# Kernel tuning notes

Measured on AMD Instinct MI355X. Metric: run time of the kernel, lower is better.

The kernel has to match this reference:

```python
import jax, jax.numpy as jnp
import numpy as np

EPS = 1e-12

def _l2norm(x):
    # F.normalize(x, dim=1): x / max(||x||_2, eps)
    n = jnp.sqrt(jnp.sum(x * x, axis=1, keepdims=True))
    return x / jnp.maximum(n, EPS)

def setup_inputs() -> dict:
    key = jax.random.key(0)
    ks = jax.random.split(key, 8)
    n_users, n_entities, channel = 100000, 100000, 128
    n_edges, n_inter, n_rel_rows = 600000, 500000, 15
    return {
        "user_emb": jax.random.normal(ks[0], (n_users, channel), dtype=jnp.float32),
        "item_emb": jax.random.normal(ks[1], (n_entities, channel), dtype=jnp.float32) * 0.1,
        "edge_index": jax.random.randint(ks[2], (2, n_edges), 0, n_entities, dtype=jnp.int64),
        "edge_type": jax.random.randint(ks[3], (n_edges,), 1, n_rel_rows + 1, dtype=jnp.int64),
        "inter_edge": jnp.stack([
            jax.random.randint(ks[4], (n_inter,), 0, n_users, dtype=jnp.int64),
            jax.random.randint(ks[5], (n_inter,), 0, n_entities, dtype=jnp.int64),
        ]),
        "inter_edge_w": jax.random.uniform(ks[6], (n_inter,), dtype=jnp.float32),
        "relation_emb": jax.random.normal(ks[7], (n_rel_rows, channel), dtype=jnp.float32) * 0.1,
        "n_hops": 2,
    }

def reference(user_emb, item_emb, edge_index, edge_type, inter_edge, inter_edge_w, relation_emb, n_hops):
    head, tail = edge_index[0], edge_index[1]
    n_entities = item_emb.shape[0]
    n_users = user_emb.shape[0]

    ent = item_emb
    for _ in range(n_hops):
        he = ent[head]                       # [E, d] gather
        te = ent[tail]                       # [E, d] gather
        re = relation_emb[edge_type - 1]     # [E, d] gather
        # scores = exp(sum(h*r*t)) then scatter_softmax over head segments
        scores = jnp.exp(jnp.sum(he * re * te, axis=1))  # [E]
        smax = jax.ops.segment_max(scores, head, num_segments=n_entities)
        e = jnp.exp(scores - smax[head])
        denom = jax.ops.segment_sum(e, head, num_segments=n_entities)
        attn = e / denom[head]
        ent = jax.ops.segment_sum(attn[:, None] * te, head, num_segments=n_entities)
        # dropout in eval mode (identity), then F.normalize
        ent = _l2norm(ent)

    u_idx, i_idx = inter_edge[0], inter_edge[1]
    item_agg = inter_edge_w[:, None] * ent[i_idx]  # [Ninter, d]
    user_agg = jax.ops.segment_sum(item_agg, u_idx, num_segments=n_users)
    return (_l2norm(user_agg), ent)
```

## Files before the change

kernel.cpp:

```cpp
#include <hip/hip_runtime.h>
#include <math.h>

#define D 128
#define EPS 1e-12f
#define SCAN_NB 128
#define SCAN_TPB 256
#define CPAD 4

template <int CTRL>
__device__ __forceinline__ float rorAdd(float v) {
    int t = __builtin_amdgcn_update_dpp(0, __float_as_int(v), CTRL, 0xF, 0xF, true);
    return v + __int_as_float(t);
}
__device__ __forceinline__ float groupSum16(float v) {
    v = rorAdd<0x121>(v);
    v = rorAdd<0x122>(v);
    v = rorAdd<0x124>(v);
    v = rorAdd<0x128>(v);
    return v;
}

__device__ __forceinline__ void unpack8(uint4 q, float* f) {
    f[0] = __uint_as_float(q.x << 16); f[1] = __uint_as_float(q.x & 0xFFFF0000u);
    f[2] = __uint_as_float(q.y << 16); f[3] = __uint_as_float(q.y & 0xFFFF0000u);
    f[4] = __uint_as_float(q.z << 16); f[5] = __uint_as_float(q.z & 0xFFFF0000u);
    f[6] = __uint_as_float(q.w << 16); f[7] = __uint_as_float(q.w & 0xFFFF0000u);
}
__device__ __forceinline__ unsigned bfpack2(float lo, float hi) {
    unsigned ul = __float_as_uint(lo), uh = __float_as_uint(hi);
    ul = (ul + 0x7FFFu + ((ul >> 16) & 1u)) >> 16;
    uh = (uh + 0x7FFFu + ((uh >> 16) & 1u)) & 0xFFFF0000u;
    return ul | uh;
}
__device__ __forceinline__ uint4 pack8(const float* f) {
    uint4 q;
    q.x = bfpack2(f[0], f[1]); q.y = bfpack2(f[2], f[3]);
    q.z = bfpack2(f[4], f[5]); q.w = bfpack2(f[6], f[7]);
    return q;
}

__global__ void k_zero(int4* __restrict__ p, int n4) {
    int i = blockIdx.x * blockDim.x + threadIdx.x;
    if (i < n4) p[i] = make_int4(0, 0, 0, 0);
}

__global__ void k_count_conv(const int* __restrict__ head, const int* __restrict__ u_idx,
                             int* __restrict__ counts_pad, int* __restrict__ rank,
                             const float* __restrict__ emb, uint4* __restrict__ mir,
                             int E, int Ninter, int N_ent, int n8) {
    int i = blockIdx.x * blockDim.x + threadIdx.x;
    int n_keys = E + Ninter;
    if (i < E) {
        rank[i] = atomicAdd(&counts_pad[(size_t)head[i] << CPAD], 1);
    } else if (i < n_keys) {
        rank[i] = atomicAdd(&counts_pad[(size_t)(N_ent + u_idx[i - E]) << CPAD], 1);
    } else if (i < n_keys + n8) {
        int c = i - n_keys;
        const float4* ip = (const float4*)emb + (size_t)c * 2;
        float4 a = ip[0], b = ip[1];
        float f[8] = {a.x, a.y, a.z, a.w, b.x, b.y, b.z, b.w};
        mir[c] = pack8(f);
    }
}

__global__ void k_count_both(const int* __restrict__ head, const int* __restrict__ u_idx,
                             int* __restrict__ counts_all, int E, int Ninter, int N_ent) {
    int i = blockIdx.x * blockDim.x + threadIdx.x;
    if (i < E) atomicAdd(&counts_all[head[i]], 1);
    else if (i < E + Ninter) atomicAdd(&counts_all[N_ent + u_idx[i - E]], 1);
}

__global__ void k_scan_block(const int* __restrict__ counts, int* __restrict__ bsum,
                             int N, int K, int shl) {
    __shared__ int lds[SCAN_TPB];
    int tid = threadIdx.x;
    int base = (blockIdx.x * SCAN_TPB + tid) * K;
    int s = 0;
    for (int k = 0; k < K; ++k) {
        int idx = base + k;
        if (idx < N) s += counts[(size_t)idx << shl];
    }
    lds[tid] = s;
    __syncthreads();
    for (int off = SCAN_TPB / 2; off > 0; off >>= 1) {
        if (tid < off) lds[tid] += lds[tid + off];
        __syncthreads();
    }
    if (tid == 0) bsum[blockIdx.x] = lds[0];
}

__global__ void k_scan_top(int* __restrict__ bsum) {
    __shared__ int lds[SCAN_NB];
    int t = threadIdx.x;
    if (t < SCAN_NB) lds[t] = bsum[t];
    __syncthreads();
    if (t == 0) {
        int run = 0;
        for (int i = 0; i < SCAN_NB; ++i) { int c = lds[i]; lds[i] = run; run += c; }
    }
    __syncthreads();
    if (t < SCAN_NB) bsum[t] = lds[t];
}

__global__ void k_scan_final(const int* __restrict__ counts, const int* __restrict__ bsum,
                             int* __restrict__ row_start, int N, int K, int shl) {
    __shared__ int lds[SCAN_TPB];
    int tid = threadIdx.x;
    int base = (blockIdx.x * SCAN_TPB + tid) * K;
    int s = 0;
    for (int k = 0; k < K; ++k) {
        int idx = base + k;
        if (idx < N) s += counts[(size_t)idx << shl];
    }
    lds[tid] = s;
    __syncthreads();
    for (int off = 1; off < SCAN_TPB; off <<= 1) {
        int v = (tid >= off) ? lds[tid - off] : 0;
        __syncthreads();
        lds[tid] += v;
        __syncthreads();
    }
    int run = lds[tid] - s + bsum[blockIdx.x];
    for (int k = 0; k < K; ++k) {
        int idx = base + k;
        if (idx <= N) {
            row_start[idx] = run;
            if (idx < N) run += counts[(size_t)idx << shl];
        }
    }
}

__global__ void k_reorder_rank(const int* __restrict__ head, const int* __restrict__ tail,
                               const int* __restrict__ etype,
                               const int* __restrict__ u_idx, const int* __restrict__ i_idx,
                               const float* __restrict__ w,
                               const int* __restrict__ rs_all, const int* __restrict__ rank,
                               int* __restrict__ packed, int2* __restrict__ riw,
                               int E, int Ninter, int N_ent) {
    int i = blockIdx.x * blockDim.x + threadIdx.x;
    if (i < E) {
        int h = head[i];
        packed[rs_all[h] + rank[i]] = tail[i] | ((etype[i] - 1) << 24);
    } else if (i < E + Ninter) {
        int k = i - E;
        int u = N_ent + u_idx[k];
        int pos = rs_all[u] + rank[i] - E;
        riw[pos] = make_int2(i_idx[k], __float_as_int(w[k]));
    }
}

__global__ void k_reorder_both(const int* __restrict__ head, const int* __restrict__ tail,
                               const int* __restrict__ etype,
                               const int* __restrict__ u_idx, const int* __restrict__ i_idx,
                               const float* __restrict__ w,
                               const int* __restrict__ rs_all, int* __restrict__ cursor,
                               int* __restrict__ packed, int2* __restrict__ riw,
                               int E, int Ninter, int N_ent) {
    int i = blockIdx.x * blockDim.x + threadIdx.x;
    if (i < E) {
        int h = head[i];
        int pos = rs_all[h] + atomicAdd(&cursor[h], 1);
        packed[pos] = tail[i] | ((etype[i] - 1) << 24);
    } else if (i < E + Ninter) {
        int k = i - E;
        int u = N_ent + u_idx[k];
        int pos = rs_all[u] + atomicAdd(&cursor[u], 1) - E;
        riw[pos] = make_int2(i_idx[k], __float_as_int(w[k]));
    }
}

__global__ void k_hop_bf16(const uint4* __restrict__ ent16,
                           const float* __restrict__ rel,
                           const int* __restrict__ rs_all,
                           const int* __restrict__ packed,
                           float* __restrict__ out_f32,
                           uint4* __restrict__ out_bf16,
                           int N) {
    int lane = threadIdx.x & 63;
    int l16 = lane & 15;
    int row = ((blockIdx.x * blockDim.x + threadIdx.x) >> 6) * 4 + (lane >> 4);
    if (row >= N) return;

    int rs = rs_all[row];
    int deg = rs_all[row + 1] - rs;

    float hv[8];
    unpack8(ent16[(size_t)row * 16 + l16], hv);

    float acc[8] = {0, 0, 0, 0, 0, 0, 0, 0};
    if (deg > 0) {
        int p = packed[rs];
        uint4 t16 = ent16[(size_t)(p & 0xFFFFFF) * 16 + l16];
        const float4* rp = (const float4*)(rel + (size_t)(((unsigned)p) >> 24) * D);
        float4 ra = rp[l16 * 2], rb = rp[l16 * 2 + 1];
        for (int j = 0; j < deg; ++j) {
            uint4 ct16 = t16;
            float4 cra = ra, crb = rb;
            if (j + 1 < deg) {
                int pn = packed[rs + j + 1];
                t16 = ent16[(size_t)(pn & 0xFFFFFF) * 16 + l16];
                rp = (const float4*)(rel + (size_t)(((unsigned)pn) >> 24) * D);
                ra = rp[l16 * 2]; rb = rp[l16 * 2 + 1];
            }
            float tv[8];
            unpack8(ct16, tv);
            float v = hv[0] * cra.x * tv[0] + hv[1] * cra.y * tv[1] +
                      hv[2] * cra.z * tv[2] + hv[3] * cra.w * tv[3] +
                      hv[4] * crb.x * tv[4] + hv[5] * crb.y * tv[5] +
                      hv[6] * crb.z * tv[6] + hv[7] * crb.w * tv[7];
            v = groupSum16(v);
            float wgt = __expf(__expf(v));
#pragma unroll
            for (int k = 0; k < 8; ++k) acc[k] += wgt * tv[k];
        }
    }

    float part = 0.f;
#pragma unroll
    for (int k = 0; k < 8; ++k) part += acc[k] * acc[k];
    float ss = groupSum16(part);
    float inv = 1.0f / fmaxf(sqrtf(ss), EPS);
#pragma unroll
    for (int k = 0; k < 8; ++k) acc[k] *= inv;

    if (out_f32) {
        float4* op = (float4*)(out_f32 + (size_t)row * D);
        op[l16 * 2]     = make_float4(acc[0], acc[1], acc[2], acc[3]);
        op[l16 * 2 + 1] = make_float4(acc[4], acc[5], acc[6], acc[7]);
    }
    if (out_bf16) out_bf16[(size_t)row * 16 + l16] = pack8(acc);
}

__global__ void k_user_bf16(const uint4* __restrict__ ent16,
                            const int* __restrict__ rs_all,
                            const int2* __restrict__ riw,
                            float* __restrict__ uout, int Nu, int N_ent, int E) {
    int lane = threadIdx.x & 63;
    int l16 = lane & 15;
    int row = ((blockIdx.x * blockDim.x + threadIdx.x) >> 6) * 4 + (lane >> 4);
    if (row >= Nu) return;

    int base = rs_all[N_ent + row];
    int deg = rs_all[N_ent + row + 1] - base;
    int rs = base - E;

    float acc[8] = {0, 0, 0, 0, 0, 0, 0, 0};
    if (deg > 0) {
        int2 pw = riw[rs];
        uint4 t16 = ent16[(size_t)pw.x * 16 + l16];
        float ww = __int_as_float(pw.y);
        for (int j = 0; j < deg; ++j) {
            uint4 ct16 = t16;
            float cw = ww;
            if (j + 1 < deg) {
                int2 pn = riw[rs + j + 1];
                t16 = ent16[(size_t)pn.x * 16 + l16];
                ww = __int_as_float(pn.y);
            }
            float tv[8];
            unpack8(ct16, tv);
#pragma unroll
            for (int k = 0; k < 8; ++k) acc[k] += cw * tv[k];
        }
    }
    float part = 0.f;
#pragma unroll
    for (int k = 0; k < 8; ++k) part += acc[k] * acc[k];
    float ss = groupSum16(part);
    float inv = 1.0f / fmaxf(sqrtf(ss), EPS);
#pragma unroll
    for (int k = 0; k < 8; ++k) acc[k] *= inv;
    float4* op = (float4*)(uout + (size_t)row * D);
    op[l16 * 2]     = make_float4(acc[0], acc[1], acc[2], acc[3]);
    op[l16 * 2 + 1] = make_float4(acc[4], acc[5], acc[6], acc[7]);
}

__global__ void k_hop_f32(const float* __restrict__ ent_in,
                          const float* __restrict__ rel,
                          const int* __restrict__ rs_all,
                          const int* __restrict__ packed,
                          float* __restrict__ ent_out, int N) {
    int lane = threadIdx.x & 63;
    int l16 = lane & 15;
    int row = ((blockIdx.x * blockDim.x + threadIdx.x) >> 6) * 4 + (lane >> 4);
    if (row >= N) return;
    int rs = rs_all[row];
    int deg = rs_all[row + 1] - rs;
    const float4* hp = (const float4*)(ent_in + (size_t)row * D);
    float4 ha = hp[l16], hb = hp[l16 + 16];
    float4 acca = make_float4(0, 0, 0, 0), accb = make_float4(0, 0, 0, 0);
    for (int j = 0; j < deg; ++j) {
        int p = packed[rs + j];
        const float4* tp = (const float4*)(ent_in + (size_t)(p & 0xFFFFFF) * D);
        const float4* rp = (const float4*)(rel + (size_t)(((unsigned)p) >> 24) * D);
        float4 ta = tp[l16], tb = tp[l16 + 16];
        float4 ra = rp[l16], rb = rp[l16 + 16];
        float v = ha.x * ra.x * ta.x + ha.y * ra.y * ta.y +
                  ha.z * ra.z * ta.z + ha.w * ra.w * ta.w +
                  hb.x * rb.x * tb.x + hb.y * rb.y * tb.y +
                  hb.z * rb.z * tb.z + hb.w * rb.w * tb.w;
        v = groupSum16(v);
        float wgt = __expf(__expf(v));
        acca.x += wgt * ta.x; acca.y += wgt * ta.y;
        acca.z += wgt * ta.z; acca.w += wgt * ta.w;
        accb.x += wgt * tb.x; accb.y += wgt * tb.y;
        accb.z += wgt * tb.z; accb.w += wgt * tb.w;
    }
    float part = acca.x * acca.x + acca.y * acca.y + acca.z * acca.z + acca.w * acca.w +
                 accb.x * accb.x + accb.y * accb.y + accb.z * accb.z + accb.w * accb.w;
    float ss = groupSum16(part);
    float inv = 1.0f / fmaxf(sqrtf(ss), EPS);
    acca.x *= inv; acca.y *= inv; acca.z *= inv; acca.w *= inv;
    accb.x *= inv; accb.y *= inv; accb.z *= inv; accb.w *= inv;
    float4* op = (float4*)(ent_out + (size_t)row * D);
    op[l16] = acca;
    op[l16 + 16] = accb;
}

__global__ void k_user_f32(const float* __restrict__ ent,
                           const int* __restrict__ rs_all,
                           const int2* __restrict__ riw,
                           float* __restrict__ uout, int Nu, int N_ent, int E) {
    int lane = threadIdx.x & 63;
    int l16 = lane & 15;
    int row = ((blockIdx.x * blockDim.x + threadIdx.x) >> 6) * 4 + (lane >> 4);
    if (row >= Nu) return;
    int base = rs_all[N_ent + row];
    int deg = rs_all[N_ent + row + 1] - base;
    int rs = base - E;
    float4 acca = make_float4(0, 0, 0, 0), accb = make_float4(0, 0, 0, 0);
    for (int j = 0; j < deg; ++j) {
        int2 pw = riw[rs + j];
        float ww = __int_as_float(pw.y);
        const float4* ip = (const float4*)(ent + (size_t)pw.x * D);
        float4 ta = ip[l16], tb = ip[l16 + 16];
        acca.x += ww * ta.x; acca.y += ww * ta.y;
        acca.z += ww * ta.z; acca.w += ww * ta.w;
        accb.x += ww * tb.x; accb.y += ww * tb.y;
        accb.z += ww * tb.z; accb.w += ww * tb.w;
    }
    float part = acca.x * acca.x + acca.y * acca.y + acca.z * acca.z + acca.w * acca.w +
                 accb.x * accb.x + accb.y * accb.y + accb.z * accb.z + accb.w * accb.w;
    float ss = groupSum16(part);
    float inv = 1.0f / fmaxf(sqrtf(ss), EPS);
    acca.x *= inv; acca.y *= inv; acca.z *= inv; acca.w *= inv;
    accb.x *= inv; accb.y *= inv; accb.z *= inv; accb.w *= inv;
    float4* op = (float4*)(uout + (size_t)row * D);
    op[l16] = acca;
    op[l16 + 16] = accb;
}

extern "C" void kernel_launch(void* const* d_in, const int* in_sizes, int n_in,
                              void* d_out, int out_size, void* d_ws, size_t ws_size,
                              hipStream_t stream) {
    const float* item_emb  = (const float*)d_in[1];
    const int*   edge_idx  = (const int*)d_in[2];
    const int*   edge_type = (const int*)d_in[3];
    const int*   inter     = (const int*)d_in[4];
    const float* inter_w   = (const float*)d_in[5];
    const float* rel       = (const float*)d_in[6];

    const int N_users = in_sizes[0] / D;
    const int N_ent   = in_sizes[1] / D;
    const int E       = in_sizes[2] / 2;
    const int Ninter  = in_sizes[5];
    const int N_tot   = N_ent + N_users;
    const int n_keys  = E + Ninter;

    float* user_out = (float*)d_out;
    float* ent_out  = (float*)d_out + (size_t)N_users * D;

    const int* head  = edge_idx;
    const int* tail  = edge_idx + E;
    const int* u_idx = inter;
    const int* i_idx = inter + Ninter;

    const int TPB = 256;
    dim3 blk(TPB);

    const size_t mir_u4 = (size_t)N_ent * 16;
    const size_t cpad_n = (size_t)N_tot << CPAD;
    uint4* mirA     = (uint4*)d_ws;
    uint4* mirB     = mirA + mir_u4;
    int2* riw       = (int2*)(mirB + mir_u4);
    int* counts_pad = (int*)(riw + Ninter);
    int* rs_all     = counts_pad + cpad_n;
    int* packed     = rs_all + N_tot + 1;
    int* bsum       = packed + E;
    int* rank       = bsum + SCAN_NB;

    size_t ints_b   = ((size_t)Ninter * 2 + cpad_n + N_tot + 1 + E + SCAN_NB + n_keys) * 4;
    size_t need_b16 = mir_u4 * 2 * 16 + ints_b;
    bool use_b16 = ws_size >= need_b16;

    int K = (N_tot + SCAN_NB * SCAN_TPB - 1) / (SCAN_NB * SCAN_TPB);
    int n8 = N_ent * (D / 8);

    if (use_b16) {
        int n4p = (int)(cpad_n / 4);
        k_zero<<<(n4p + TPB - 1) / TPB, blk, 0, stream>>>((int4*)counts_pad, n4p);
        k_count_conv<<<(n_keys + n8 + TPB - 1) / TPB, blk, 0, stream>>>(
            head, u_idx, counts_pad, rank, item_emb, mirA, E, Ninter, N_ent, n8);
        k_scan_block<<<SCAN_NB, SCAN_TPB, 0, stream>>>(counts_pad, bsum, N_tot, K, CPAD);
        k_scan_top<<<1, SCAN_TPB, 0, stream>>>(bsum);
        k_scan_final<<<SCAN_NB, SCAN_TPB, 0, stream>>>(counts_pad, bsum, rs_all, N_tot, K, CPAD);
        k_reorder_rank<<<(n_keys + TPB - 1) / TPB, blk, 0, stream>>>(
            head, tail, edge_type, u_idx, i_idx, inter_w,
            rs_all, rank, packed, riw, E, Ninter, N_ent);

        int grid_rows  = (N_ent + 15) / 16;
        int grid_users = (N_users + 15) / 16;
        k_hop_bf16<<<grid_rows, blk, 0, stream>>>(
            mirA, rel, rs_all, packed, nullptr, mirB, N_ent);
        k_hop_bf16<<<grid_rows, blk, 0, stream>>>(
            mirB, rel, rs_all, packed, ent_out, mirA, N_ent);
        k_user_bf16<<<grid_users, blk, 0, stream>>>(
            mirA, rs_all, riw, user_out, N_users, N_ent, E);
    } else {
        int2* riw2       = (int2*)d_ws;
        int* counts_all  = (int*)(riw2 + Ninter);
        int* rs2         = counts_all + N_tot;
        int* packed2     = rs2 + N_tot + 1;
        int* bsum2       = packed2 + E;
        int n4 = N_tot / 4;
        k_zero<<<(n4 + TPB - 1) / TPB, blk, 0, stream>>>((int4*)counts_all, n4);
        k_count_both<<<(n_keys + TPB - 1) / TPB, blk, 0, stream>>>(
            head, u_idx, counts_all, E, Ninter, N_ent);
        k_scan_block<<<SCAN_NB, SCAN_TPB, 0, stream>>>(counts_all, bsum2, N_tot, K, 0);
        k_scan_top<<<1, SCAN_TPB, 0, stream>>>(bsum2);
        k_scan_final<<<SCAN_NB, SCAN_TPB, 0, stream>>>(counts_all, bsum2, rs2, N_tot, K, 0);
        k_zero<<<(n4 + TPB - 1) / TPB, blk, 0, stream>>>((int4*)counts_all, n4);
        k_reorder_both<<<(n_keys + TPB - 1) / TPB, blk, 0, stream>>>(
            head, tail, edge_type, u_idx, i_idx, inter_w,
            rs2, counts_all, packed2, riw2, E, Ninter, N_ent);
        int grid_rows  = (N_ent + 15) / 16;
        int grid_users = (N_users + 15) / 16;
        float* ent_mid = user_out;
        k_hop_f32<<<grid_rows, blk, 0, stream>>>(item_emb, rel, rs2, packed2, ent_mid, N_ent);
        k_hop_f32<<<grid_rows, blk, 0, stream>>>(ent_mid, rel, rs2, packed2, ent_out, N_ent);
        k_user_f32<<<grid_users, blk, 0, stream>>>(
            ent_out, rs2, riw2, user_out, N_users, N_ent, E);
    }
}
```

Measured before the change: 208.5 us.

## Split entity and user CSR builds and overlap user build with hop kernels

Result: no change. 209.7 us (+0.6%).

```diff
diff --git a/kernel.cpp b/kernel.cpp
--- a/kernel.cpp
+++ b/kernel.cpp
@@ -5,7 +5,6 @@
 #define EPS 1e-12f
 #define SCAN_NB 128
 #define SCAN_TPB 256
-#define CPAD 4
 
 template <int CTRL>
 __device__ __forceinline__ float rorAdd(float v) {
@@ -44,18 +43,23 @@
     if (i < n4) p[i] = make_int4(0, 0, 0, 0);
 }
 
-__global__ void k_count_conv(const int* __restrict__ head, const int* __restrict__ u_idx,
-                             int* __restrict__ counts_pad, int* __restrict__ rank,
-                             const float* __restrict__ emb, uint4* __restrict__ mir,
-                             int E, int Ninter, int N_ent, int n8) {
+__global__ void k_count_e(const int* __restrict__ head, int* __restrict__ counts_ent,
+                          int* __restrict__ rank_e, int E) {
     int i = blockIdx.x * blockDim.x + threadIdx.x;
-    int n_keys = E + Ninter;
+    if (i < E) rank_e[i] = atomicAdd(&counts_ent[head[i]], 1);
+}
+
+__global__ void k_reorder_conv(const int* __restrict__ head, const int* __restrict__ tail,
+                               const int* __restrict__ etype,
+                               const int* __restrict__ rs_ent, const int* __restrict__ rank_e,
+                               int* __restrict__ packed,
+                               const float* __restrict__ emb, uint4* __restrict__ mir,
+                               int E, int n8) {
+    int i = blockIdx.x * blockDim.x + threadIdx.x;
     if (i < E) {
-        rank[i] = atomicAdd(&counts_pad[(size_t)head[i] << CPAD], 1);
-    } else if (i < n_keys) {
-        rank[i] = atomicAdd(&counts_pad[(size_t)(N_ent + u_idx[i - E]) << CPAD], 1);
-    } else if (i < n_keys + n8) {
-        int c = i - n_keys;
+        packed[rs_ent[head[i]] + rank_e[i]] = tail[i] | ((etype[i] - 1) << 24);
+    } else if (i < E + n8) {
+        int c = i - E;
         const float4* ip = (const float4*)emb + (size_t)c * 2;
         float4 a = ip[0], b = ip[1];
         float f[8] = {a.x, a.y, a.z, a.w, b.x, b.y, b.z, b.w};
@@ -63,23 +67,13 @@
     }
 }
 
-__global__ void k_count_both(const int* __restrict__ head, const int* __restrict__ u_idx,
-                             int* __restrict__ counts_all, int E, int Ninter, int N_ent) {
-    int i = blockIdx.x * blockDim.x + threadIdx.x;
-    if (i < E) atomicAdd(&counts_all[head[i]], 1);
-    else if (i < E + Ninter) atomicAdd(&counts_all[N_ent + u_idx[i - E]], 1);
-}
-
 __global__ void k_scan_block(const int* __restrict__ counts, int* __restrict__ bsum,
-                             int N, int K, int shl) {
+                             int N, int K) {
     __shared__ int lds[SCAN_TPB];
     int tid = threadIdx.x;
     int base = (blockIdx.x * SCAN_TPB + tid) * K;
     int s = 0;
-    for (int k = 0; k < K; ++k) {
-        int idx = base + k;
-        if (idx < N) s += counts[(size_t)idx << shl];
-    }
+    for (int k = 0; k < K; ++k) { int idx = base + k; if (idx < N) s += counts[idx]; }
     lds[tid] = s;
     __syncthreads();
     for (int off = SCAN_TPB / 2; off > 0; off >>= 1) {
@@ -103,15 +97,12 @@
 }
 
 __global__ void k_scan_final(const int* __restrict__ counts, const int* __restrict__ bsum,
-                             int* __restrict__ row_start, int N, int K, int shl) {
+                             int* __restrict__ row_start, int N, int K) {
     __shared__ int lds[SCAN_TPB];
     int tid = threadIdx.x;
     int base = (blockIdx.x * SCAN_TPB + tid) * K;
     int s = 0;
-    for (int k = 0; k < K; ++k) {
-        int idx = base + k;
-        if (idx < N) s += counts[(size_t)idx << shl];
-    }
+    for (int k = 0; k < K; ++k) { int idx = base + k; if (idx < N) s += counts[idx]; }
     lds[tid] = s;
     __syncthreads();
     for (int off = 1; off < SCAN_TPB; off <<= 1) {
@@ -125,64 +116,26 @@
         int idx = base + k;
         if (idx <= N) {
             row_start[idx] = run;
-            if (idx < N) run += counts[(size_t)idx << shl];
+            if (idx < N) run += counts[idx];
         }
     }
 }
 
-__global__ void k_reorder_rank(const int* __restrict__ head, const int* __restrict__ tail,
-                               const int* __restrict__ etype,
-                               const int* __restrict__ u_idx, const int* __restrict__ i_idx,
-                               const float* __restrict__ w,
-                               const int* __restrict__ rs_all, const int* __restrict__ rank,
-                               int* __restrict__ packed, int2* __restrict__ riw,
-                               int E, int Ninter, int N_ent) {
-    int i = blockIdx.x * blockDim.x + threadIdx.x;
-    if (i < E) {
-        int h = head[i];
-        packed[rs_all[h] + rank[i]] = tail[i] | ((etype[i] - 1) << 24);
-    } else if (i < E + Ninter) {
-        int k = i - E;
-        int u = N_ent + u_idx[k];
-        int pos = rs_all[u] + rank[i] - E;
-        riw[pos] = make_int2(i_idx[k], __float_as_int(w[k]));
-    }
-}
-
-__global__ void k_reorder_both(const int* __restrict__ head, const int* __restrict__ tail,
-                               const int* __restrict__ etype,
-                               const int* __restrict__ u_idx, const int* __restrict__ i_idx,
-                               const float* __restrict__ w,
-                               const int* __restrict__ rs_all, int* __restrict__ cursor,
-                               int* __restrict__ packed, int2* __restrict__ riw,
-                               int E, int Ninter, int N_ent) {
-    int i = blockIdx.x * blockDim.x + threadIdx.x;
-    if (i < E) {
-        int h = head[i];
-        int pos = rs_all[h] + atomicAdd(&cursor[h], 1);
-        packed[pos] = tail[i] | ((etype[i] - 1) << 24);
-    } else if (i < E + Ninter) {
-        int k = i - E;
-        int u = N_ent + u_idx[k];
-        int pos = rs_all[u] + atomicAdd(&cursor[u], 1) - E;
-        riw[pos] = make_int2(i_idx[k], __float_as_int(w[k]));
-    }
-}
-
-__global__ void k_hop_bf16(const uint4* __restrict__ ent16,
-                           const float* __restrict__ rel,
-                           const int* __restrict__ rs_all,
-                           const int* __restrict__ packed,
-                           float* __restrict__ out_f32,
-                           uint4* __restrict__ out_bf16,
-                           int N) {
-    int lane = threadIdx.x & 63;
+
+__device__ __forceinline__ void hop_body(const uint4* __restrict__ ent16,
+                                         const float* __restrict__ rel,
+                                         const int* __restrict__ rs_ent,
+                                         const int* __restrict__ packed,
+                                         float* __restrict__ out_f32,
+                                         uint4* __restrict__ out_bf16,
+                                         int N, int tid_g) {
+    int lane = tid_g & 63;
     int l16 = lane & 15;
-    int row = ((blockIdx.x * blockDim.x + threadIdx.x) >> 6) * 4 + (lane >> 4);
+    int row = (tid_g >> 6) * 4 + (lane >> 4);
     if (row >= N) return;
 
-    int rs = rs_all[row];
-    int deg = rs_all[row + 1] - rs;
+    int rs = rs_ent[row];
+    int deg = rs_ent[row + 1] - rs;
 
     float hv[8];
     unpack8(ent16[(size_t)row * 16 + l16], hv);
@@ -231,18 +184,56 @@
     if (out_bf16) out_bf16[(size_t)row * 16 + l16] = pack8(acc);
 }
 
+__global__ void k_hop1_ucount(const uint4* __restrict__ ent16,
+                              const float* __restrict__ rel,
+                              const int* __restrict__ rs_ent,
+                              const int* __restrict__ packed,
+                              uint4* __restrict__ out_bf16,
+                              const int* __restrict__ u_idx,
+                              int* __restrict__ counts_usr, int* __restrict__ rank_u,
+                              int N, int HOPT, int Ninter) {
+    int tid_g = blockIdx.x * blockDim.x + threadIdx.x;
+    if (tid_g < HOPT) {
+        hop_body(ent16, rel, rs_ent, packed, nullptr, out_bf16, N, tid_g);
+    } else {
+        int k = tid_g - HOPT;
+        if (k < Ninter) rank_u[k] = atomicAdd(&counts_usr[u_idx[k]], 1);
+    }
+}
+
+__global__ void k_hop2_ureorder(const uint4* __restrict__ ent16,
+                                const float* __restrict__ rel,
+                                const int* __restrict__ rs_ent,
+                                const int* __restrict__ packed,
+                                float* __restrict__ out_f32, uint4* __restrict__ out_bf16,
+                                const int* __restrict__ u_idx, const int* __restrict__ i_idx,
+                                const float* __restrict__ w,
+                                const int* __restrict__ rs_usr, const int* __restrict__ rank_u,
+                                int2* __restrict__ riw,
+                                int N, int HOPT, int Ninter) {
+    int tid_g = blockIdx.x * blockDim.x + threadIdx.x;
+    if (tid_g < HOPT) {
+        hop_body(ent16, rel, rs_ent, packed, out_f32, out_bf16, N, tid_g);
+    } else {
+        int k = tid_g - HOPT;
+        if (k < Ninter) {
+            int u = u_idx[k];
+            riw[rs_usr[u] + rank_u[k]] = make_int2(i_idx[k], __float_as_int(w[k]));
+        }
+    }
+}
+
 __global__ void k_user_bf16(const uint4* __restrict__ ent16,
-                            const int* __restrict__ rs_all,
+                            const int* __restrict__ rs_usr,
                             const int2* __restrict__ riw,
-                            float* __restrict__ uout, int Nu, int N_ent, int E) {
+                            float* __restrict__ uout, int Nu) {
     int lane = threadIdx.x & 63;
     int l16 = lane & 15;
     int row = ((blockIdx.x * blockDim.x + threadIdx.x) >> 6) * 4 + (lane >> 4);
     if (row >= Nu) return;
 
-    int base = rs_all[N_ent + row];
-    int deg = rs_all[N_ent + row + 1] - base;
-    int rs = base - E;
+    int rs = rs_usr[row];
+    int deg = rs_usr[row + 1] - rs;
 
     float acc[8] = {0, 0, 0, 0, 0, 0, 0, 0};
     if (deg > 0) {
@@ -273,6 +264,33 @@
     float4* op = (float4*)(uout + (size_t)row * D);
     op[l16 * 2]     = make_float4(acc[0], acc[1], acc[2], acc[3]);
     op[l16 * 2 + 1] = make_float4(acc[4], acc[5], acc[6], acc[7]);
+}
+
+__global__ void k_count_both(const int* __restrict__ head, const int* __restrict__ u_idx,
+                             int* __restrict__ counts_all, int E, int Ninter, int N_ent) {
+    int i = blockIdx.x * blockDim.x + threadIdx.x;
+    if (i < E) atomicAdd(&counts_all[head[i]], 1);
+    else if (i < E + Ninter) atomicAdd(&counts_all[N_ent + u_idx[i - E]], 1);
+}
+
+__global__ void k_reorder_both(const int* __restrict__ head, const int* __restrict__ tail,
+                               const int* __restrict__ etype,
+                               const int* __restrict__ u_idx, const int* __restrict__ i_idx,
+                               const float* __restrict__ w,
+                               const int* __restrict__ rs_all, int* __restrict__ cursor,
+                               int* __restrict__ packed, int2* __restrict__ riw,
+                               int E, int Ninter, int N_ent) {
+    int i = blockIdx.x * blockDim.x + threadIdx.x;
+    if (i < E) {
+        int h = head[i];
+        int pos = rs_all[h] + atomicAdd(&cursor[h], 1);
+        packed[pos] = tail[i] | ((etype[i] - 1) << 24);
+    } else if (i < E + Ninter) {
+        int k = i - E;
+        int u = N_ent + u_idx[k];
+        int pos = rs_all[u] + atomicAdd(&cursor[u], 1) - E;
+        riw[pos] = make_int2(i_idx[k], __float_as_int(w[k]));
+    }
 }
 
 __global__ void k_hop_f32(const float* __restrict__ ent_in,
@@ -379,56 +397,70 @@
     dim3 blk(TPB);
 
     const size_t mir_u4 = (size_t)N_ent * 16;
-    const size_t cpad_n = (size_t)N_tot << CPAD;
     uint4* mirA     = (uint4*)d_ws;
     uint4* mirB     = mirA + mir_u4;
     int2* riw       = (int2*)(mirB + mir_u4);
-    int* counts_pad = (int*)(riw + Ninter);
-    int* rs_all     = counts_pad + cpad_n;
-    int* packed     = rs_all + N_tot + 1;
-    int* bsum       = packed + E;
-    int* rank       = bsum + SCAN_NB;
-
-    size_t ints_b   = ((size_t)Ninter * 2 + cpad_n + N_tot + 1 + E + SCAN_NB + n_keys) * 4;
+    int* counts_ent = (int*)(riw + Ninter);
+    int* counts_usr = counts_ent + N_ent;
+    int* rs_ent     = counts_usr + N_users;
+    int* rs_usr     = rs_ent + N_ent + 1;
+    int* bsumE      = rs_usr + N_users + 1;
+    int* bsumU      = bsumE + SCAN_NB;
+    int* rank_e     = bsumU + SCAN_NB;
+    int* rank_u     = rank_e + E;
+    int* packed     = rank_u + Ninter;
+
+    size_t ints_b   = ((size_t)Ninter * 2 + N_tot + N_tot + 2 + 2 * SCAN_NB +
+                       E + Ninter + E) * 4;
     size_t need_b16 = mir_u4 * 2 * 16 + ints_b;
     bool use_b16 = ws_size >= need_b16;
 
-    int K = (N_tot + SCAN_NB * SCAN_TPB - 1) / (SCAN_NB * SCAN_TPB);
     int n8 = N_ent * (D / 8);
 
     if (use_b16) {
-        int n4p = (int)(cpad_n / 4);
-        k_zero<<<(n4p + TPB - 1) / TPB, blk, 0, stream>>>((int4*)counts_pad, n4p);
-        k_count_conv<<<(n_keys + n8 + TPB - 1) / TPB, blk, 0, stream>>>(
-            head, u_idx, counts_pad, rank, item_emb, mirA, E, Ninter, N_ent, n8);
-        k_scan_block<<<SCAN_NB, SCAN_TPB, 0, stream>>>(counts_pad, bsum, N_tot, K, CPAD);
-        k_scan_top<<<1, SCAN_TPB, 0, stream>>>(bsum);
-        k_scan_final<<<SCAN_NB, SCAN_TPB, 0, stream>>>(counts_pad, bsum, rs_all, N_tot, K, CPAD);
-        k_reorder_rank<<<(n_keys + TPB - 1) / TPB, blk, 0, stream>>>(
-            head, tail, edge_type, u_idx, i_idx, inter_w,
-            rs_all, rank, packed, riw, E, Ninter, N_ent);
-
-        int grid_rows  = (N_ent + 15) / 16;
-        int grid_users = (N_users + 15) / 16;
-        k_hop_bf16<<<grid_rows, blk, 0, stream>>>(
-            mirA, rel, rs_all, packed, nullptr, mirB, N_ent);
-        k_hop_bf16<<<grid_rows, blk, 0, stream>>>(
-            mirB, rel, rs_all, packed, ent_out, mirA, N_ent);
-        k_user_bf16<<<grid_users, blk, 0, stream>>>(
-            mirA, rs_all, riw, user_out, N_users, N_ent, E);
+        int K_e = (N_ent + SCAN_NB * SCAN_TPB - 1) / (SCAN_NB * SCAN_TPB);
+        int K_u = (N_users + SCAN_NB * SCAN_TPB - 1) / (SCAN_NB * SCAN_TPB);
+        int HOPT = ((N_ent + 3) / 4) * 64;
+
+        int n4 = N_tot / 4;
+        k_zero<<<(n4 + TPB - 1) / TPB, blk, 0, stream>>>((int4*)counts_ent, n4);
+
+        k_count_e<<<(E + TPB - 1) / TPB, blk, 0, stream>>>(head, counts_ent, rank_e, E);
+        k_scan_block<<<SCAN_NB, SCAN_TPB, 0, stream>>>(counts_ent, bsumE, N_ent, K_e);
+        k_scan_top<<<1, SCAN_TPB, 0, stream>>>(bsumE);
+        k_scan_final<<<SCAN_NB, SCAN_TPB, 0, stream>>>(counts_ent, bsumE, rs_ent, N_ent, K_e);
+        k_reorder_conv<<<(E + n8 + TPB - 1) / TPB, blk, 0, stream>>>(
+            head, tail, edge_type, rs_ent, rank_e, packed, item_emb, mirA, E, n8);
+
+        k_hop1_ucount<<<(HOPT + Ninter + TPB - 1) / TPB, blk, 0, stream>>>(
+            mirA, rel, rs_ent, packed, mirB, u_idx, counts_usr, rank_u,
+            N_ent, HOPT, Ninter);
+
+        k_scan_block<<<SCAN_NB, SCAN_TPB, 0, stream>>>(counts_usr, bsumU, N_users, K_u);
+        k_scan_top<<<1, SCAN_TPB, 0, stream>>>(bsumU);
+        k_scan_final<<<SCAN_NB, SCAN_TPB, 0, stream>>>(counts_usr, bsumU, rs_usr, N_users, K_u);
+
+        k_hop2_ureorder<<<(HOPT + Ninter + TPB - 1) / TPB, blk, 0, stream>>>(
+            mirB, rel, rs_ent, packed, ent_out, mirA,
+            u_idx, i_idx, inter_w, rs_usr, rank_u, riw,
+            N_ent, HOPT, Ninter);
+
+        k_user_bf16<<<(N_users + 15) / 16, blk, 0, stream>>>(
+            mirA, rs_usr, riw, user_out, N_users);
     } else {
         int2* riw2       = (int2*)d_ws;
         int* counts_all  = (int*)(riw2 + Ninter);
         int* rs2         = counts_all + N_tot;
         int* packed2     = rs2 + N_tot + 1;
         int* bsum2       = packed2 + E;
+        int K = (N_tot + SCAN_NB * SCAN_TPB - 1) / (SCAN_NB * SCAN_TPB);
         int n4 = N_tot / 4;
         k_zero<<<(n4 + TPB - 1) / TPB, blk, 0, stream>>>((int4*)counts_all, n4);
         k_count_both<<<(n_keys + TPB - 1) / TPB, blk, 0, stream>>>(
             head, u_idx, counts_all, E, Ninter, N_ent);
-        k_scan_block<<<SCAN_NB, SCAN_TPB, 0, stream>>>(counts_all, bsum2, N_tot, K, 0);
+        k_scan_block<<<SCAN_NB, SCAN_TPB, 0, stream>>>(counts_all, bsum2, N_tot, K);
         k_scan_top<<<1, SCAN_TPB, 0, stream>>>(bsum2);
-        k_scan_final<<<SCAN_NB, SCAN_TPB, 0, stream>>>(counts_all, bsum2, rs2, N_tot, K, 0);
+        k_scan_final<<<SCAN_NB, SCAN_TPB, 0, stream>>>(counts_all, bsum2, rs2, N_tot, K);
         k_zero<<<(n4 + TPB - 1) / TPB, blk, 0, stream>>>((int4*)counts_all, n4);
         k_reorder_both<<<(n_keys + TPB - 1) / TPB, blk, 0, stream>>>(
             head, tail, edge_type, u_idx, i_idx, inter_w,
```
